# Kernel optimization log

Measured on AMD Instinct MI355X. Metric: run time of the kernel, lower is better.

Reference implementation:

```python
import jax, jax.numpy as jnp
import numpy as np

D_MODEL = 1024
N_HEADS = 16
D_K = D_MODEL // N_HEADS
B, L = 4, 2048


def setup_inputs() -> dict:
    key = jax.random.key(0)
    ks = jax.random.split(key, 9)
    s = 1.0 / np.sqrt(D_MODEL)
    return {
        "x": jax.random.normal(ks[0], (B, L, D_MODEL), dtype=jnp.float32),
        "Wq": jax.random.normal(ks[1], (D_MODEL, D_MODEL), dtype=jnp.float32) * s,
        "bq": jax.random.normal(ks[2], (D_MODEL,), dtype=jnp.float32) * 0.01,
        "Wk": jax.random.normal(ks[3], (D_MODEL, D_MODEL), dtype=jnp.float32) * s,
        "bk": jax.random.normal(ks[4], (D_MODEL,), dtype=jnp.float32) * 0.01,
        "Wv": jax.random.normal(ks[5], (D_MODEL, D_MODEL), dtype=jnp.float32) * s,
        "bv": jax.random.normal(ks[6], (D_MODEL,), dtype=jnp.float32) * 0.01,
        "Wo": jax.random.normal(ks[7], (D_MODEL, D_MODEL), dtype=jnp.float32) * s,
        "bo": jax.random.normal(ks[8], (D_MODEL,), dtype=jnp.float32) * 0.01,
    }


def reference(x, Wq, bq, Wk, bk, Wv, bv, Wo, bo):
    b, l, d = x.shape
    scale = jnp.asarray(np.sqrt(D_K), x.dtype)
    # project and split heads: [B, H, L, d_k]
    def heads(w, bias):
        p = x @ w.T + bias
        return p.reshape(b, l, N_HEADS, D_K).transpose(0, 2, 1, 3)
    Q = heads(Wq, bq)
    K = heads(Wk, bk)
    V = heads(Wv, bv)
    scores = jnp.einsum("bhqd,bhkd->bhqk", Q, K) / scale
    scores = jnp.clip(scores, -100.0, 100.0)
    attn = jax.nn.softmax(scores, axis=-1)  # dropout is identity in eval
    ctx = jnp.einsum("bhqk,bhkd->bhqd", attn, V)
    ctx = ctx.transpose(0, 2, 1, 3).reshape(b, l, d)
    return ctx @ Wo.T + bo
```

## Files before the change

### kernel.cpp

```cpp
#include <hip/hip_runtime.h>
#include <stdint.h>

#define L_SEQ   2048
#define DM      1024
#define NH      16
#define DK      64
#define BATCH   4
#define M_TOK   (BATCH * L_SEQ)

typedef __attribute__((ext_vector_type(8))) short bf16x8;
typedef __attribute__((ext_vector_type(4))) float f32x4;
typedef __attribute__((ext_vector_type(16))) float f32x16;
typedef __attribute__((ext_vector_type(4))) unsigned int u32x4;

typedef __attribute__((address_space(1))) void void_g;
typedef __attribute__((address_space(3))) void void_l;

#define EXP2F(x) __builtin_amdgcn_exp2f(x)

__device__ __forceinline__ unsigned short f2bf(float f) {
  unsigned int u = __builtin_bit_cast(unsigned int, f);
  u += 0x7FFFu + ((u >> 16) & 1u);
  return (unsigned short)(u >> 16);
}

__global__ void cvt_f32_bf16(const float* __restrict__ src,
                             unsigned short* __restrict__ dst, int n4) {
  int i = blockIdx.x * blockDim.x + threadIdx.x;
  int stride = gridDim.x * blockDim.x;
  for (; i < n4; i += stride) {
    float4 v = ((const float4*)src)[i];
    ushort4 o;
    o.x = f2bf(v.x); o.y = f2bf(v.y); o.z = f2bf(v.z); o.w = f2bf(v.w);
    ((ushort4*)dst)[i] = o;
  }
}

__global__ void cvt_w4(const float* __restrict__ s0, const float* __restrict__ s1,
                       const float* __restrict__ s2, const float* __restrict__ s3,
                       unsigned short* __restrict__ dst) {
  int i = blockIdx.x * blockDim.x + threadIdx.x;
  int sel = i >> 18, j = i & 0x3FFFF;
  const float* s = sel == 0 ? s0 : sel == 1 ? s1 : sel == 2 ? s2 : s3;
  float4 v = ((const float4*)s)[j];
  ushort4 o;
  o.x = f2bf(v.x); o.y = f2bf(v.y); o.z = f2bf(v.z); o.w = f2bf(v.w);
  ((ushort4*)(dst + (size_t)sel * DM * DM))[j] = o;
}

#define GBK 32
#define NKT (DM / GBK)
#define AT32 (128 * GBK)

template <int NW, int NCH>
__device__ __forceinline__ void stage32(
    const unsigned short* __restrict__ S, unsigned short* buf,
    int row0, int k0, int t) {
  const int l = t & 63, w = t >> 6;
  const int su = (l & 3) ^ ((l >> 3) & 3);
  const int rl = l >> 2;
#pragma unroll
  for (int r = 0; r < NCH / NW; ++r) {
    const int c = r * NW + w;
    __builtin_amdgcn_global_load_lds(
        (const void_g*)(S + (size_t)(row0 + c * 16 + rl) * DM + k0 + su * 8),
        (void_l*)(buf + c * 512), 16, 0, 0);
  }
}

__device__ __forceinline__ bf16x8 frag_ld32(const unsigned short* base, int R, int u) {
  return *(const bf16x8*)(base + R * 32 + ((u ^ ((R >> 1) & 3)) * 8));
}

template <int EPI, int BN_, int NW>
__global__ __launch_bounds__(NW * 64, EPI == 0 ? 4 : 3) void gemm8(
    const unsigned short* __restrict__ A,
    const unsigned short* __restrict__ Bw,
    const float* __restrict__ b0, const float* __restrict__ b1,
    const float* __restrict__ b2, float qscale,
    void* __restrict__ out) {
  constexpr int BUFE = (128 + BN_) * GBK;
  constexpr int BCH = BN_ / 16;
  __shared__ unsigned short L[3 * BUFE];

  const int tidx = threadIdx.x;
  const int wid = tidx >> 6, lane = tidx & 63;
  constexpr int WN = NW / 2;
  const int wm = wid / WN, wn = wid % WN;
  const int lr = lane & 15, lg4 = lane >> 4;

  int wg = blockIdx.y * gridDim.x + blockIdx.x;
  int nwg = gridDim.x * gridDim.y;
  int swz = (wg & 7) * (nwg >> 3) + (wg >> 3);
  const int tm = (swz / gridDim.x) * 128, tn = (swz % gridDim.x) * BN_;

  f32x4 acc[4][4];
#pragma unroll
  for (int m = 0; m < 4; ++m)
#pragma unroll
    for (int n = 0; n < 4; ++n) acc[m][n] = (f32x4)0.0f;

  stage32<NW, 8>(A, L, tm, 0, tidx);
  stage32<NW, BCH>(Bw, L + AT32, tn, 0, tidx);
  stage32<NW, 8>(A, L + BUFE, tm, GBK, tidx);
  stage32<NW, BCH>(Bw, L + BUFE + AT32, tn, GBK, tidx);
  if constexpr (EPI == 0) asm volatile("s_waitcnt vmcnt(3)" ::: "memory");
  else                    asm volatile("s_waitcnt vmcnt(4)" ::: "memory");
  __builtin_amdgcn_s_barrier();

  for (int i = 0; i < NKT; ++i) {
    unsigned short* cb = L + (i % 3) * BUFE;
    unsigned short* nb = L + ((i + 2) % 3) * BUFE;
    const bool pf = (i + 2 < NKT);

    bf16x8 a[4], b[4];
#pragma unroll
    for (int m = 0; m < 4; ++m)
      a[m] = frag_ld32(cb, wm * 64 + m * 16 + lr, lg4);
#pragma unroll
    for (int n = 0; n < 4; ++n)
      b[n] = frag_ld32(cb + AT32, wn * 64 + n * 16 + lr, lg4);

    if (pf) {
      stage32<NW, 8>(A, nb, tm, (i + 2) * GBK, tidx);
      stage32<NW, BCH>(Bw, nb + AT32, tn, (i + 2) * GBK, tidx);
    }

    asm volatile("s_waitcnt lgkmcnt(0)" ::: "memory");
    __builtin_amdgcn_s_setprio(1);
#pragma unroll
    for (int m = 0; m < 4; ++m)
#pragma unroll
      for (int n = 0; n < 4; ++n)
        acc[m][n] = __builtin_amdgcn_mfma_f32_16x16x32_bf16(a[m], b[n], acc[m][n], 0, 0, 0);
    __builtin_amdgcn_s_setprio(0);

    if (pf) {
      if constexpr (EPI == 0) asm volatile("s_waitcnt vmcnt(3)" ::: "memory");
      else                    asm volatile("s_waitcnt vmcnt(4)" ::: "memory");
    } else {
      asm volatile("s_waitcnt vmcnt(0)" ::: "memory");
    }
    __builtin_amdgcn_s_barrier();
  }

  if (EPI == 1) {
    float* o = (float*)out;
#pragma unroll
    for (int m = 0; m < 4; ++m) {
      int row0 = tm + wm * 64 + m * 16 + lg4 * 4;
#pragma unroll
      for (int n = 0; n < 4; ++n) {
        int col = tn + wn * 64 + n * 16 + lr;
        float bc = b0[col];
#pragma unroll
        for (int jj = 0; jj < 4; ++jj)
          o[(size_t)(row0 + jj) * DM + col] = acc[m][n][jj] + bc;
      }
    }
  } else {
    const int sel = tn >> 10;
    const float* bias = sel == 0 ? b0 : sel == 1 ? b1 : b2;
    const float scl = sel == 0 ? qscale : 1.0f;
    unsigned short* dst = (unsigned short*)out + (size_t)sel * (8u << 20);
    unsigned short* C = L;
    const int bb = tm >> 11, l0 = tm & 2047;
    const int tnl = tn & 1023;
    constexpr int LST = BN_ + 8;
    constexpr int CPR = BN_ / 8;
    constexpr int ITR = 128 * CPR / (NW * 64);

    if (sel < 2) {
#pragma unroll
      for (int m = 0; m < 4; ++m) {
        int row0 = wm * 64 + m * 16 + lg4 * 4;
#pragma unroll
        for (int n = 0; n < 4; ++n) {
          int col = wn * 64 + n * 16 + lr;
          float bc = bias[tnl + col];
#pragma unroll
          for (int jj = 0; jj < 4; ++jj)
            C[(row0 + jj) * LST + col] = f2bf((acc[m][n][jj] + bc) * scl);
        }
      }
      __syncthreads();
#pragma unroll
      for (int j = 0; j < ITR; ++j) {
        int c = j * NW * 64 + tidx;
        int ll = c / CPR, colc = (c % CPR) * 8;
        bf16x8 v = *(const bf16x8*)&C[ll * LST + colc];
        int c10 = tnl + colc;
        int h = c10 >> 6, dd = c10 & 63;
        *(bf16x8*)&dst[(((size_t)bb * NH + h) * L_SEQ + (l0 + ll)) * DK + dd] = v;
      }
    } else {
#pragma unroll
      for (int m = 0; m < 4; ++m) {
        int row0 = wm * 64 + m * 16 + lg4 * 4;
#pragma unroll
        for (int n = 0; n < 4; ++n) {
          int col = wn * 64 + n * 16 + lr;
          float bc = bias[tnl + col];
          ushort4 pk;
          pk.x = f2bf(acc[m][n][0] + bc);
          pk.y = f2bf(acc[m][n][1] + bc);
          pk.z = f2bf(acc[m][n][2] + bc);
          pk.w = f2bf(acc[m][n][3] + bc);
          *(ushort4*)&C[col * 136 + row0] = pk;
        }
      }
      __syncthreads();
      constexpr int ITV = BN_ * 16 / (NW * 64);
#pragma unroll
      for (int j = 0; j < ITV; ++j) {
        int c = j * NW * 64 + tidx;
        int ddl = c >> 4, tk = (c & 15) * 8;
        bf16x8 v = *(const bf16x8*)&C[ddl * 136 + tk];
        int c10 = tnl + ddl;
        int h = c10 >> 6, dd = c10 & 63;
        *(bf16x8*)&dst[(((size_t)bb * NH + h) * DK + dd) * L_SEQ + (l0 + tk)] = v;
      }
    }
  }
}

#define KVB 64
#define LDK 68
#define NTILE (L_SEQ / KVB)
#define FIXM  32.0f

__device__ __forceinline__ bf16x8 lds_frag(const unsigned short* p) {
  uint2 a = *(const uint2*)p;
  uint2 b = *(const uint2*)(p + 4);
  u32x4 t = {a.x, a.y, b.x, b.y};
  return __builtin_bit_cast(bf16x8, t);
}

__device__ __forceinline__ void lds_st16(unsigned short* p, uint4 v) {
  *(uint2*)p = make_uint2(v.x, v.y);
  *(uint2*)(p + 4) = make_uint2(v.z, v.w);
}

__device__ __forceinline__ unsigned cvtpk(float a, float b) {
  unsigned r;
  asm("v_cvt_pk_bf16_f32 %0, %1, %2" : "=v"(r) : "v"(a), "v"(b));
  return r;
}

__device__ __forceinline__ void pl32swap(unsigned& a, unsigned& b) {
  unsigned sa = (unsigned)__shfl_xor((int)a, 32);
  unsigned sb = (unsigned)__shfl_xor((int)b, 32);
  int hi = (threadIdx.x & 63) >> 5;
  unsigned na = hi ? sb : a;
  unsigned nb = hi ? b : sa;
  a = na; b = nb;
}

__device__ __forceinline__ void xpair32(float x, float& lo, float& hi2) {
  unsigned a = __builtin_bit_cast(unsigned, x), b = a;
  pl32swap(a, b);
  lo = __builtin_bit_cast(float, a);
  hi2 = __builtin_bit_cast(float, b);
}

#define MFMA32(a, b, c) __builtin_amdgcn_mfma_f32_32x32x16_bf16(a, b, c, 0, 0, 0)

__global__ __launch_bounds__(256, 4) void flash_attn(
    const unsigned short* __restrict__ Qg,
    const unsigned short* __restrict__ Kg,
    const unsigned short* __restrict__ VTg,
    unsigned short* __restrict__ ctx) {
  __shared__ unsigned short Ks[2][64 * LDK];
  __shared__ unsigned short Vs[2][64 * LDK];

  const int bh = blockIdx.x, b = bh >> 4, h = bh & 15;
  const int q0 = blockIdx.y * 128;
  const int tid = threadIdx.x;
  const int w = tid >> 6, lane = tid & 63;
  const int l31 = lane & 31, hi = lane >> 5;
  const size_t head = (size_t)bh * (L_SEQ * DK);

  const int srow = w * 16 + (lane >> 2);
  const int scol = (lane & 3) * 16;

  bf16x8 qf[4];
  {
    const unsigned short* qp = Qg + head + (size_t)(q0 + w * 32 + l31) * DK + hi * 8;
#pragma unroll
    for (int ks = 0; ks < 4; ++ks) qf[ks] = *(const bf16x8*)(qp + ks * 16);
  }

  f32x16 o[2];
  o[0] = (f32x16)0.0f; o[1] = (f32x16)0.0f;
  float lq = 0.0f;

  {
    const unsigned short* kp = Kg + head + (size_t)srow * DK + scol;
    uint4 k0 = *(const uint4*)kp, k1 = *(const uint4*)(kp + 8);
    const unsigned short* vp = VTg + head + (size_t)srow * L_SEQ + scol;
    uint4 v0 = *(const uint4*)vp, v1 = *(const uint4*)(vp + 8);
    lds_st16(Ks[0] + srow * LDK + scol, k0);
    lds_st16(Ks[0] + srow * LDK + scol + 8, k1);
    lds_st16(Vs[0] + srow * LDK + scol, v0);
    lds_st16(Vs[0] + srow * LDK + scol + 8, v1);
  }
  __syncthreads();

  int cur = 0;
  for (int t = 0; t < NTILE; ++t) {
    uint4 kr0, kr1, vr0, vr1;
    const int kv0n = (t + 1) * KVB;
    if (t + 1 < NTILE) {
      const unsigned short* kp = Kg + head + (size_t)(kv0n + srow) * DK + scol;
      kr0 = *(const uint4*)kp; kr1 = *(const uint4*)(kp + 8);
    }

    f32x16 s0 = (f32x16)(-FIXM), s1 = (f32x16)(-FIXM);
#pragma unroll
    for (int ks = 0; ks < 4; ++ks) {
      bf16x8 k0 = lds_frag(Ks[cur] + l31 * LDK + ks * 16 + hi * 8);
      s0 = MFMA32(k0, qf[ks], s0);
      bf16x8 k1 = lds_frag(Ks[cur] + (32 + l31) * LDK + ks * 16 + hi * 8);
      s1 = MFMA32(k1, qf[ks], s1);
    }

#pragma unroll
    for (int r = 0; r < 16; ++r) {
      s0[r] = EXP2F(s0[r]);
      s1[r] = EXP2F(s1[r]);
    }
    {
      float l4[4];
#pragma unroll
      for (int r = 0; r < 4; ++r)
        l4[r] = ((s0[r] + s0[r + 4]) + (s0[r + 8] + s0[r + 12]))
              + ((s1[r] + s1[r + 4]) + (s1[r + 8] + s1[r + 12]));
      lq += (l4[0] + l4[1]) + (l4[2] + l4[3]);
    }

    bf16x8 pa[4];
#pragma unroll
    for (int ks = 0; ks < 4; ++ks) {
      const int s8 = (ks & 1) * 8;
      const f32x16 sv = (ks < 2) ? s0 : s1;
      unsigned uA0 = cvtpk(sv[s8 + 0], sv[s8 + 1]);
      unsigned uA1 = cvtpk(sv[s8 + 2], sv[s8 + 3]);
      unsigned uB0 = cvtpk(sv[s8 + 4], sv[s8 + 5]);
      unsigned uB1 = cvtpk(sv[s8 + 6], sv[s8 + 7]);
      pl32swap(uA0, uB0);
      pl32swap(uA1, uB1);
      u32x4 tt = {uA0, uA1, uB0, uB1};
      pa[ks] = __builtin_bit_cast(bf16x8, tt);
    }

    if (t + 1 < NTILE) {
      const unsigned short* vp = VTg + head + (size_t)srow * L_SEQ + kv0n + scol;
      vr0 = *(const uint4*)vp; vr1 = *(const uint4*)(vp + 8);
    }

#pragma unroll
    for (int jb = 0; jb < 2; ++jb)
#pragma unroll
      for (int ks = 0; ks < 4; ++ks) {
        bf16x8 vf = lds_frag(Vs[cur] + (32 * jb + l31) * LDK + ks * 16 + hi * 8);
        o[jb] = MFMA32(vf, pa[ks], o[jb]);
      }

    if (t + 1 < NTILE) {
      lds_st16(Ks[cur ^ 1] + srow * LDK + scol, kr0);
      lds_st16(Ks[cur ^ 1] + srow * LDK + scol + 8, kr1);
      lds_st16(Vs[cur ^ 1] + srow * LDK + scol, vr0);
      lds_st16(Vs[cur ^ 1] + srow * LDK + scol + 8, vr1);
    }
    __syncthreads();
    cur ^= 1;
  }

  {
    float a, c;
    xpair32(lq, a, c);
    float inv = 1.0f / (a + c);
    const int tok = q0 + w * 32 + l31;
    size_t base = ((size_t)b * L_SEQ + tok) * DM + h * DK;
#pragma unroll
    for (int jb = 0; jb < 2; ++jb)
#pragma unroll
      for (int c2 = 0; c2 < 4; ++c2) {
        ushort4 pk;
        pk.x = f2bf(o[jb][4 * c2 + 0] * inv);
        pk.y = f2bf(o[jb][4 * c2 + 1] * inv);
        pk.z = f2bf(o[jb][4 * c2 + 2] * inv);
        pk.w = f2bf(o[jb][4 * c2 + 3] * inv);
        *(ushort4*)&ctx[base + jb * 32 + c2 * 8 + hi * 4] = pk;
      }
  }
}

extern "C" void kernel_launch(void* const* d_in, const int* in_sizes, int n_in,
                              void* d_out, int out_size, void* d_ws, size_t ws_size,
                              hipStream_t stream) {
  (void)in_sizes; (void)n_in; (void)out_size; (void)ws_size;
  const float* x  = (const float*)d_in[0];
  const float* Wq = (const float*)d_in[1];
  const float* bq = (const float*)d_in[2];
  const float* Wk = (const float*)d_in[3];
  const float* bk = (const float*)d_in[4];
  const float* Wv = (const float*)d_in[5];
  const float* bv = (const float*)d_in[6];
  const float* Wo = (const float*)d_in[7];
  const float* bo = (const float*)d_in[8];

  char* ws = (char*)d_ws;
  unsigned short* xb  = (unsigned short*)(ws);
  unsigned short* wqb = (unsigned short*)(ws + (16ull << 20));
  unsigned short* wob = (unsigned short*)(ws + (22ull << 20));
  unsigned short* Qb  = (unsigned short*)(ws + (24ull << 20));
  unsigned short* Kb  = (unsigned short*)(ws + (40ull << 20));
  unsigned short* VTb = (unsigned short*)(ws + (56ull << 20));
  unsigned short* ctx = xb;

  cvt_f32_bf16<<<2048, 256, 0, stream>>>(x, xb, M_TOK * DM / 4);
  cvt_w4<<<4096, 256, 0, stream>>>(Wq, Wk, Wv, Wo, wqb);

  gemm8<0, 256, 8><<<dim3(3 * DM / 256, M_TOK / 128), 512, 0, stream>>>(
      xb, wqb, bq, bk, bv, 0.1803368801f, Qb);

  dim3 ga(BATCH * NH, L_SEQ / 128);
  flash_attn<<<ga, 256, 0, stream>>>(Qb, Kb, VTb, ctx);

  gemm8<1, 128, 4><<<dim3(DM / 128, M_TOK / 128), 256, 0, stream>>>(
      ctx, wob, bo, nullptr, nullptr, 1.0f, d_out);
}
```

Baseline: 188.0 us.

## Split KV sequence across two wave groups in flash attention and merge via LDS

Doubles the flash attention block to 512 threads, with two halves of four waves each handling half of the KV sequence in 32-key tiles. A final LDS reduction adds the second half's partial outputs and row sums into the first half before normalisation. The aim is more waves in flight per query tile to hide latency, at the cost of smaller MFMA tiles per iteration, more barriers and an extra LDS merge step. The fixed-max softmax means no rescaling is needed when the halves are combined.

```diff
diff --git a/kernel.cpp b/kernel.cpp
--- a/kernel.cpp
+++ b/kernel.cpp
@@ -224,10 +224,15 @@
   }
 }
 
-#define KVB 64
-#define LDK 68
-#define NTILE (L_SEQ / KVB)
-#define FIXM  32.0f
+#define KVB2 32
+#define LDK2 68
+#define LDV2 36
+#define NT2  32
+#define KS_E (KVB2 * LDK2)
+#define VS_E (64 * LDV2)
+#define HALF_E (2 * (KS_E + VS_E))
+#define FIXM 32.0f
+#define OMST 66
 
 __device__ __forceinline__ bf16x8 lds_frag(const unsigned short* p) {
   uint2 a = *(const uint2*)p;
@@ -265,27 +270,32 @@
 
 #define MFMA32(a, b, c) __builtin_amdgcn_mfma_f32_32x32x16_bf16(a, b, c, 0, 0, 0)
 
-__global__ __launch_bounds__(256, 4) void flash_attn(
+__global__ __launch_bounds__(512, 6) void flash_attn(
     const unsigned short* __restrict__ Qg,
     const unsigned short* __restrict__ Kg,
     const unsigned short* __restrict__ VTg,
     unsigned short* __restrict__ ctx) {
-  __shared__ unsigned short Ks[2][64 * LDK];
-  __shared__ unsigned short Vs[2][64 * LDK];
-
+  __shared__ unsigned short Lds[2 * HALF_E];
+
+  const int tid = threadIdx.x;
+  const int w = tid >> 6, lane = tid & 63;
+  const int half = w >> 2, wl = w & 3;
+  const int l31 = lane & 31, hi = lane >> 5;
   const int bh = blockIdx.x, b = bh >> 4, h = bh & 15;
   const int q0 = blockIdx.y * 128;
-  const int tid = threadIdx.x;
-  const int w = tid >> 6, lane = tid & 63;
-  const int l31 = lane & 31, hi = lane >> 5;
   const size_t head = (size_t)bh * (L_SEQ * DK);
-
-  const int srow = w * 16 + (lane >> 2);
-  const int scol = (lane & 3) * 16;
+  const int kvbase = half * (L_SEQ / 2);
+
+  unsigned short* Ks = Lds + half * HALF_E;
+  unsigned short* Vs = Ks + 2 * KS_E;
+
+  const int ht = tid & 255;
+  const int krow = ht >> 3, kcol = (ht & 7) * 8;
+  const int vrow = ht >> 2, vcol = (ht & 3) * 8;
 
   bf16x8 qf[4];
   {
-    const unsigned short* qp = Qg + head + (size_t)(q0 + w * 32 + l31) * DK + hi * 8;
+    const unsigned short* qp = Qg + head + (size_t)(q0 + wl * 32 + l31) * DK + hi * 8;
 #pragma unroll
     for (int ks = 0; ks < 4; ++ks) qf[ks] = *(const bf16x8*)(qp + ks * 16);
   }
@@ -295,102 +305,101 @@
   float lq = 0.0f;
 
   {
-    const unsigned short* kp = Kg + head + (size_t)srow * DK + scol;
-    uint4 k0 = *(const uint4*)kp, k1 = *(const uint4*)(kp + 8);
-    const unsigned short* vp = VTg + head + (size_t)srow * L_SEQ + scol;
-    uint4 v0 = *(const uint4*)vp, v1 = *(const uint4*)(vp + 8);
-    lds_st16(Ks[0] + srow * LDK + scol, k0);
-    lds_st16(Ks[0] + srow * LDK + scol + 8, k1);
-    lds_st16(Vs[0] + srow * LDK + scol, v0);
-    lds_st16(Vs[0] + srow * LDK + scol + 8, v1);
+    uint4 kr = *(const uint4*)(Kg + head + (size_t)(kvbase + krow) * DK + kcol);
+    uint4 vr = *(const uint4*)(VTg + head + (size_t)vrow * L_SEQ + kvbase + vcol);
+    lds_st16(Ks + krow * LDK2 + kcol, kr);
+    lds_st16(Vs + vrow * LDV2 + vcol, vr);
   }
   __syncthreads();
 
   int cur = 0;
-  for (int t = 0; t < NTILE; ++t) {
-    uint4 kr0, kr1, vr0, vr1;
-    const int kv0n = (t + 1) * KVB;
-    if (t + 1 < NTILE) {
-      const unsigned short* kp = Kg + head + (size_t)(kv0n + srow) * DK + scol;
-      kr0 = *(const uint4*)kp; kr1 = *(const uint4*)(kp + 8);
-    }
-
-    f32x16 s0 = (f32x16)(-FIXM), s1 = (f32x16)(-FIXM);
+  for (int t = 0; t < NT2; ++t) {
+    uint4 kr, vr;
+    const int kvn = kvbase + (t + 1) * KVB2;
+    if (t + 1 < NT2) {
+      kr = *(const uint4*)(Kg + head + (size_t)(kvn + krow) * DK + kcol);
+      vr = *(const uint4*)(VTg + head + (size_t)vrow * L_SEQ + kvn + vcol);
+    }
+
+    f32x16 s = (f32x16)(-FIXM);
 #pragma unroll
     for (int ks = 0; ks < 4; ++ks) {
-      bf16x8 k0 = lds_frag(Ks[cur] + l31 * LDK + ks * 16 + hi * 8);
-      s0 = MFMA32(k0, qf[ks], s0);
-      bf16x8 k1 = lds_frag(Ks[cur] + (32 + l31) * LDK + ks * 16 + hi * 8);
-      s1 = MFMA32(k1, qf[ks], s1);
-    }
-
-#pragma unroll
-    for (int r = 0; r < 16; ++r) {
-      s0[r] = EXP2F(s0[r]);
-      s1[r] = EXP2F(s1[r]);
-    }
+      bf16x8 kf = lds_frag(Ks + cur * KS_E + l31 * LDK2 + ks * 16 + hi * 8);
+      s = MFMA32(kf, qf[ks], s);
+    }
+
+#pragma unroll
+    for (int r = 0; r < 16; ++r) s[r] = EXP2F(s[r]);
     {
       float l4[4];
 #pragma unroll
       for (int r = 0; r < 4; ++r)
-        l4[r] = ((s0[r] + s0[r + 4]) + (s0[r + 8] + s0[r + 12]))
-              + ((s1[r] + s1[r + 4]) + (s1[r + 8] + s1[r + 12]));
+        l4[r] = (s[r] + s[r + 4]) + (s[r + 8] + s[r + 12]);
       lq += (l4[0] + l4[1]) + (l4[2] + l4[3]);
     }
 
-    bf16x8 pa[4];
-#pragma unroll
-    for (int ks = 0; ks < 4; ++ks) {
-      const int s8 = (ks & 1) * 8;
-      const f32x16 sv = (ks < 2) ? s0 : s1;
-      unsigned uA0 = cvtpk(sv[s8 + 0], sv[s8 + 1]);
-      unsigned uA1 = cvtpk(sv[s8 + 2], sv[s8 + 3]);
-      unsigned uB0 = cvtpk(sv[s8 + 4], sv[s8 + 5]);
-      unsigned uB1 = cvtpk(sv[s8 + 6], sv[s8 + 7]);
+    bf16x8 pa[2];
+#pragma unroll
+    for (int ks = 0; ks < 2; ++ks) {
+      const int s8 = ks * 8;
+      unsigned uA0 = cvtpk(s[s8 + 0], s[s8 + 1]);
+      unsigned uA1 = cvtpk(s[s8 + 2], s[s8 + 3]);
+      unsigned uB0 = cvtpk(s[s8 + 4], s[s8 + 5]);
+      unsigned uB1 = cvtpk(s[s8 + 6], s[s8 + 7]);
       pl32swap(uA0, uB0);
       pl32swap(uA1, uB1);
       u32x4 tt = {uA0, uA1, uB0, uB1};
       pa[ks] = __builtin_bit_cast(bf16x8, tt);
     }
 
-    if (t + 1 < NTILE) {
-      const unsigned short* vp = VTg + head + (size_t)srow * L_SEQ + kv0n + scol;
-      vr0 = *(const uint4*)vp; vr1 = *(const uint4*)(vp + 8);
-    }
-
 #pragma unroll
     for (int jb = 0; jb < 2; ++jb)
 #pragma unroll
-      for (int ks = 0; ks < 4; ++ks) {
-        bf16x8 vf = lds_frag(Vs[cur] + (32 * jb + l31) * LDK + ks * 16 + hi * 8);
+      for (int ks = 0; ks < 2; ++ks) {
+        bf16x8 vf = lds_frag(Vs + cur * VS_E + (32 * jb + l31) * LDV2 + ks * 16 + hi * 8);
         o[jb] = MFMA32(vf, pa[ks], o[jb]);
       }
 
-    if (t + 1 < NTILE) {
-      lds_st16(Ks[cur ^ 1] + srow * LDK + scol, kr0);
-      lds_st16(Ks[cur ^ 1] + srow * LDK + scol + 8, kr1);
-      lds_st16(Vs[cur ^ 1] + srow * LDK + scol, vr0);
-      lds_st16(Vs[cur ^ 1] + srow * LDK + scol + 8, vr1);
+    if (t + 1 < NT2) {
+      lds_st16(Ks + (cur ^ 1) * KS_E + krow * LDK2 + kcol, kr);
+      lds_st16(Vs + (cur ^ 1) * VS_E + vrow * LDV2 + vcol, vr);
     }
     __syncthreads();
     cur ^= 1;
   }
 
-  {
+  float* oL = (float*)Lds;
+  float* lqL = oL + 128 * OMST;
+  const int qr = wl * 32 + l31;
+
+  if (half == 1) {
+#pragma unroll
+    for (int jb = 0; jb < 2; ++jb)
+#pragma unroll
+      for (int c2 = 0; c2 < 4; ++c2)
+#pragma unroll
+        for (int j = 0; j < 4; ++j)
+          oL[qr * OMST + (jb * 32 + c2 * 8 + hi * 4 + j)] = o[jb][4 * c2 + j];
+    lqL[qr * 2 + hi] = lq;
+  }
+  __syncthreads();
+  if (half == 0) {
     float a, c;
     xpair32(lq, a, c);
-    float inv = 1.0f / (a + c);
-    const int tok = q0 + w * 32 + l31;
+    float inv = 1.0f / (a + c + lqL[qr * 2] + lqL[qr * 2 + 1]);
+    const int tok = q0 + qr;
     size_t base = ((size_t)b * L_SEQ + tok) * DM + h * DK;
 #pragma unroll
     for (int jb = 0; jb < 2; ++jb)
 #pragma unroll
       for (int c2 = 0; c2 < 4; ++c2) {
         ushort4 pk;
-        pk.x = f2bf(o[jb][4 * c2 + 0] * inv);
-        pk.y = f2bf(o[jb][4 * c2 + 1] * inv);
-        pk.z = f2bf(o[jb][4 * c2 + 2] * inv);
-        pk.w = f2bf(o[jb][4 * c2 + 3] * inv);
+#pragma unroll
+        for (int j = 0; j < 4; ++j) {
+          float v = (o[jb][4 * c2 + j] +
+                     oL[qr * OMST + (jb * 32 + c2 * 8 + hi * 4 + j)]) * inv;
+          ((unsigned short*)&pk)[j] = f2bf(v);
+        }
         *(ushort4*)&ctx[base + jb * 32 + c2 * 8 + hi * 4] = pk;
       }
   }
@@ -426,7 +435,7 @@
       xb, wqb, bq, bk, bv, 0.1803368801f, Qb);
 
   dim3 ga(BATCH * NH, L_SEQ / 128);
-  flash_attn<<<ga, 256, 0, stream>>>(Qb, Kb, VTb, ctx);
+  flash_attn<<<ga, 512, 0, stream>>>(Qb, Kb, VTb, ctx);
 
   gemm8<1, 128, 4><<<dim3(DM / 128, M_TOK / 128), 256, 0, stream>>>(
       ctx, wob, bo, nullptr, nullptr, 1.0f, d_out);
```

After: 620.3 us. +229.9%, slower.
